# Performance work log

Hardware: AMD Instinct MI355X
Metric: run time of the kernel (lower is better)

Reference implementation:

```python
import jax, jax.numpy as jnp
import numpy as np

T, B, D_IN, D_HID, D_OUT = 512, 64, 512, 512, 512


def setup_inputs() -> dict:
    key = jax.random.key(0)
    k_x, k_xh, k_hh, k_o = jax.random.split(key, 4)
    return {
        "x": jax.random.normal(k_x, (T, B, D_IN), dtype=jnp.float32),
        "xh": jax.random.normal(k_xh, (D_IN, D_HID), dtype=jnp.float32) * 0.01,
        "hh": jax.random.normal(k_hh, (D_HID, D_HID), dtype=jnp.float32) * 0.01,
        "hb": jnp.zeros((D_HID,), dtype=jnp.float32),
        "o": jax.random.normal(k_o, (D_HID, D_OUT), dtype=jnp.float32) * 0.01,
        "h0": jnp.zeros((1, D_HID), dtype=jnp.float32),
    }


def reference(x, xh, hh, hb, o, h0):
    # Elman RNN (training branch): h_t = relu(x_t @ xh + h_{t-1} @ hh + hb); y_t = h_t @ o
    # h starts as (1, hid) and broadcasts to (B, hid) at step 1, as in the torch code.
    batch = x.shape[1]
    h_init = jnp.broadcast_to(h0, (batch, h0.shape[1]))

    def step(h, xi):  # xi: [B, D_IN], h: [B, D_HID]
        h = jax.nn.relu(xi @ xh + h @ hh + hb)
        return h, h @ o  # y: [B, D_OUT]

    _, ys = jax.lax.scan(step, h_init, x)
    return ys  # [T, B, D_OUT] (stacked version of the torch list of outputs)
```

## Files before the change

### kernel.cpp

```cpp
#include <hip/hip_runtime.h>
#include <hip/hip_bf16.h>

#define TSTEPS 512
#define BATCH  64
#define DIM    512
#define NWG    8

using short8 = __attribute__((ext_vector_type(8))) short;
using f32x4  = __attribute__((ext_vector_type(4))) float;

__device__ __forceinline__ unsigned short f2bf(float f) {
    unsigned u = __builtin_bit_cast(unsigned, f);
    unsigned r = (u + 0x7FFFu + ((u >> 16) & 1u)) >> 16;
    return (unsigned short)r;
}

__global__ void conv_oT(const float* __restrict__ src, unsigned short* __restrict__ dst) {
    __shared__ float tile[32][33];
    const int bx = blockIdx.x * 32, by = blockIdx.y * 32;
    const int tx = threadIdx.x & 31, ty = threadIdx.x >> 5;
#pragma unroll
    for (int k = 0; k < 32; k += 8)
        tile[ty + k][tx] = src[(size_t)(by + ty + k) * DIM + bx + tx];
    __syncthreads();
#pragma unroll
    for (int k = 0; k < 32; k += 8)
        dst[(size_t)(bx + ty + k) * DIM + by + tx] = f2bf(tile[tx][ty + k]);
}

__global__ __launch_bounds__(256) void gemm_xw(
    const float* __restrict__ X, const float* __restrict__ W,
    const float* __restrict__ bias, float* __restrict__ Out)
{
    __shared__ float As[16][68];
    __shared__ float Bs[16][68];
    const int tid = threadIdx.x;
    const int m0 = blockIdx.x * 64, n0 = blockIdx.y * 64;
    const int tx = tid & 15, ty = tid >> 4;
    float acc[4][4] = {};
    for (int k0 = 0; k0 < DIM; k0 += 16) {
        {
            int r = tid >> 2, c = (tid & 3) * 4;
            float4 v = *reinterpret_cast<const float4*>(X + (size_t)(m0 + r) * DIM + k0 + c);
            As[c + 0][r] = v.x; As[c + 1][r] = v.y; As[c + 2][r] = v.z; As[c + 3][r] = v.w;
        }
        {
            int r = tid >> 4, c = (tid & 15) * 4;
            float4 v = *reinterpret_cast<const float4*>(W + (size_t)(k0 + r) * DIM + n0 + c);
            Bs[r][c + 0] = v.x; Bs[r][c + 1] = v.y; Bs[r][c + 2] = v.z; Bs[r][c + 3] = v.w;
        }
        __syncthreads();
#pragma unroll
        for (int k = 0; k < 16; ++k) {
            float4 a = *reinterpret_cast<const float4*>(&As[k][ty * 4]);
            float4 b = *reinterpret_cast<const float4*>(&Bs[k][tx * 4]);
            float av[4] = {a.x, a.y, a.z, a.w};
            float bv[4] = {b.x, b.y, b.z, b.w};
#pragma unroll
            for (int i = 0; i < 4; ++i)
#pragma unroll
                for (int j = 0; j < 4; ++j)
                    acc[i][j] = fmaf(av[i], bv[j], acc[i][j]);
        }
        __syncthreads();
    }
    float4 bv = *reinterpret_cast<const float4*>(bias + n0 + tx * 4);
    const float badd[4] = {bv.x, bv.y, bv.z, bv.w};
    float4* Out4 = reinterpret_cast<float4*>(Out);
    const size_t base = (((size_t)blockIdx.x * 4 + (ty & 3)) * 4 + (ty >> 2)) * DIM + n0 + tx * 4;
#pragma unroll
    for (int j = 0; j < 4; ++j) {
        float4 v;
        v.x = acc[0][j] + badd[j]; v.y = acc[1][j] + badd[j];
        v.z = acc[2][j] + badd[j]; v.w = acc[3][j] + badd[j];
        Out4[base + j] = v;
    }
}

__global__ __launch_bounds__(256, 1) void rnn_scan(
    const float* __restrict__ hh, const float* __restrict__ xwb,
    const float* __restrict__ h0, unsigned long long* __restrict__ histU,
    unsigned int* __restrict__ flags)
{
    const int tid  = threadIdx.x;
    const int wg   = blockIdx.x;
    const int lane = tid & 63;
    const int wv   = __builtin_amdgcn_readfirstlane(tid >> 6);
    const int ln15 = lane & 15, kg = lane >> 4;
    const int colw = wg * 64 + wv * 16 + ln15;

    __shared__ unsigned long long hsU[BATCH * DIM / 4];

    short8 Bhh[16];
#pragma unroll
    for (int kk = 0; kk < 16; ++kk) {
        short8 bh;
#pragma unroll
        for (int j = 0; j < 8; ++j) {
            int k = kk * 32 + kg * 8 + j;
            bh[j] = (short)f2bf(hh[(size_t)k * DIM + colw]);
        }
        Bhh[kk] = bh;
    }

    {
        unsigned long long* dst = histU + wv * 2048 + lane;
#pragma unroll 4
        for (int i = 0; i < 32; ++i) {
            float4 f = *reinterpret_cast<const float4*>(h0 + ((i & 1) << 8) + lane * 4);
            unsigned long long v = (unsigned long long)f2bf(f.x)
                | ((unsigned long long)f2bf(f.y) << 16)
                | ((unsigned long long)f2bf(f.z) << 32)
                | ((unsigned long long)f2bf(f.w) << 48);
            __hip_atomic_store(dst + i * 64, v, __ATOMIC_RELAXED, __HIP_MEMORY_SCOPE_AGENT);
        }
    }
    __builtin_amdgcn_fence(__ATOMIC_RELEASE, "agent");
    __syncthreads();

    const float4* xw4 = reinterpret_cast<const float4*>(xwb);
    f32x4 xwr[4];
#pragma unroll
    for (int m = 0; m < 4; ++m) {
        float4 v = xw4[(((size_t)0 * 4 + kg) * 4 + m) * DIM + colw];
        xwr[m] = f32x4{v.x, v.y, v.z, v.w};
    }

    for (int t = 0; t < TSTEPS; ++t) {
        {
            const unsigned long long* src = histU + (size_t)t * 8192 + wv * 2048 + lane;
#pragma unroll
            for (int ii = 0; ii < 32; ii += 8) {
                unsigned long long v[8];
#pragma unroll
                for (int j = 0; j < 8; ++j)
                    v[j] = __hip_atomic_load(src + (ii + j) * 64, __ATOMIC_RELAXED, __HIP_MEMORY_SCOPE_AGENT);
#pragma unroll
                for (int j = 0; j < 8; ++j) {
                    int i = ii + j;
                    int row = (wv << 4) + (i >> 1);
                    int byte = ((row << 10) + ((i & 1) << 9) + (lane << 3)) ^ ((row & 7) << 4);
                    hsU[byte >> 3] = v[j];
                }
            }
        }
        __syncthreads();

        f32x4 acch[4];
#pragma unroll
        for (int m = 0; m < 4; ++m) acch[m] = f32x4{0.f, 0.f, 0.f, 0.f};
#pragma unroll
        for (int kk = 0; kk < 16; ++kk) {
#pragma unroll
            for (int m = 0; m < 4; ++m) {
                int row = m * 16 + ln15;
                int byte = ((row << 10) + (kk << 6) + (kg << 4)) ^ ((row & 7) << 4);
                short8 a = *reinterpret_cast<const short8*>(
                    reinterpret_cast<const char*>(hsU) + byte);
                acch[m] = __builtin_amdgcn_mfma_f32_16x16x32_bf16(a, Bhh[kk], acch[m], 0, 0, 0);
            }
        }

        {
            unsigned short* hdst = reinterpret_cast<unsigned short*>(histU + (size_t)(t + 1) * 8192);
#pragma unroll
            for (int m = 0; m < 4; ++m)
#pragma unroll
                for (int r = 0; r < 4; ++r) {
                    int row = m * 16 + kg * 4 + r;
                    float hn = xwr[m][r] + acch[m][r];
                    hn = hn > 0.f ? hn : 0.f;
                    __hip_atomic_store(hdst + (size_t)row * DIM + colw, f2bf(hn),
                                       __ATOMIC_RELAXED, __HIP_MEMORY_SCOPE_AGENT);
                }
        }
        __builtin_amdgcn_fence(__ATOMIC_RELEASE, "agent");
        __syncthreads();
        if (tid == 0)
            __hip_atomic_store(&flags[wg], (unsigned)(t + 1),
                               __ATOMIC_RELEASE, __HIP_MEMORY_SCOPE_AGENT);

        if (t < TSTEPS - 1) {
#pragma unroll
            for (int m = 0; m < 4; ++m) {
                float4 v = xw4[(((size_t)(t + 1) * 4 + kg) * 4 + m) * DIM + colw];
                xwr[m] = f32x4{v.x, v.y, v.z, v.w};
            }
            if (wv == 0) {
                for (;;) {
                    unsigned f = __hip_atomic_load(&flags[lane & (NWG - 1)],
                                                   __ATOMIC_RELAXED, __HIP_MEMORY_SCOPE_AGENT);
                    if (!__any(f < (unsigned)(t + 1))) break;
                    __builtin_amdgcn_s_sleep(1);
                }
            }
            __syncthreads();
        }
    }
}

__global__ __launch_bounds__(256) void gemm_y(
    const unsigned short* __restrict__ A,
    const unsigned short* __restrict__ Bt,
    float* __restrict__ Out)
{
    __shared__ unsigned short As[128 * 40];
    __shared__ unsigned short Bs[128 * 40];
    const int tid = threadIdx.x;
    const int m0 = blockIdx.x * 128, n0 = blockIdx.y * 128;
    const int lane = tid & 63, wv = tid >> 6;
    const int ln15 = lane & 15, kg = lane >> 4;
    const int wr = (wv >> 1) * 64, wc = (wv & 1) * 64;

    f32x4 acc[4][4];
#pragma unroll
    for (int m = 0; m < 4; ++m)
#pragma unroll
        for (int n = 0; n < 4; ++n) acc[m][n] = f32x4{0.f, 0.f, 0.f, 0.f};

    const int sr = tid & 127;
    for (int k0 = 0; k0 < DIM; k0 += 32) {
        const unsigned short* g = (tid < 128)
            ? A  + (size_t)(m0 + sr) * DIM + k0
            : Bt + (size_t)(n0 + sr) * DIM + k0;
        unsigned short* s = (tid < 128) ? &As[sr * 40] : &Bs[sr * 40];
        ulonglong2 v0 = reinterpret_cast<const ulonglong2*>(g)[0];
        ulonglong2 v1 = reinterpret_cast<const ulonglong2*>(g)[1];
        ulonglong2 v2 = reinterpret_cast<const ulonglong2*>(g)[2];
        ulonglong2 v3 = reinterpret_cast<const ulonglong2*>(g)[3];
        __syncthreads();
        reinterpret_cast<ulonglong2*>(s)[0] = v0;
        reinterpret_cast<ulonglong2*>(s)[1] = v1;
        reinterpret_cast<ulonglong2*>(s)[2] = v2;
        reinterpret_cast<ulonglong2*>(s)[3] = v3;
        __syncthreads();
        short8 af[4], bf[4];
#pragma unroll
        for (int m = 0; m < 4; ++m)
            af[m] = *reinterpret_cast<const short8*>(&As[(wr + m * 16 + ln15) * 40 + kg * 8]);
#pragma unroll
        for (int n = 0; n < 4; ++n)
            bf[n] = *reinterpret_cast<const short8*>(&Bs[(wc + n * 16 + ln15) * 40 + kg * 8]);
#pragma unroll
        for (int m = 0; m < 4; ++m)
#pragma unroll
            for (int n = 0; n < 4; ++n)
                acc[m][n] = __builtin_amdgcn_mfma_f32_16x16x32_bf16(af[m], bf[n], acc[m][n], 0, 0, 0);
    }
#pragma unroll
    for (int m = 0; m < 4; ++m)
#pragma unroll
        for (int n = 0; n < 4; ++n)
#pragma unroll
            for (int r = 0; r < 4; ++r) {
                int row = m0 + wr + m * 16 + kg * 4 + r;
                int col = n0 + wc + n * 16 + ln15;
                Out[(size_t)row * DIM + col] = acc[m][n][r];
            }
}

extern "C" void kernel_launch(void* const* d_in, const int* in_sizes, int n_in,
                              void* d_out, int out_size, void* d_ws, size_t ws_size,
                              hipStream_t stream) {
    const float* x  = (const float*)d_in[0];
    const float* xh = (const float*)d_in[1];
    const float* hh = (const float*)d_in[2];
    const float* hb = (const float*)d_in[3];
    const float* o  = (const float*)d_in[4];
    const float* h0 = (const float*)d_in[5];
    float* out = (float*)d_out;

    unsigned int* flags = (unsigned int*)d_ws;
    unsigned long long* histU = (unsigned long long*)((char*)d_ws + 4096);
    unsigned short* oT = (unsigned short*)((char*)d_ws + 4096 + (size_t)513 * 65536);

    (void)hipMemsetAsync(d_ws, 0, 256, stream);
    conv_oT<<<dim3(16, 16), 256, 0, stream>>>(o, oT);
    gemm_xw<<<dim3(512, 8), 256, 0, stream>>>(x, xh, hb, out);
    rnn_scan<<<NWG, 256, 0, stream>>>(hh, out, h0, histU, flags);
    gemm_y<<<dim3(256, 4), 256, 0, stream>>>(
        (const unsigned short*)histU + 32768, oT, out);
}
```

Baseline: 2.492 ms.

## Use bf16 MFMA for input projection GEMM and relax scan release fences

Replaces the fp32 FMA input-projection GEMM with a 128x128-tile bf16 MFMA kernel, pre-transposing and converting xh to bf16 with the existing transpose kernel. Separately, the recurrent scan swaps agent-scope release fences and the release flag store for an s_waitcnt vmcnt(0) plus a relaxed flag store, to shorten each step's synchronization latency. The GEMM change loses precision on x@xh, and the weaker memory ordering relies on hardware behaviour for cross-workgroup visibility of the hidden-state stores.

```diff
diff --git a/kernel.cpp b/kernel.cpp
--- a/kernel.cpp
+++ b/kernel.cpp
@@ -15,7 +15,7 @@
     return (unsigned short)r;
 }
 
-__global__ void conv_oT(const float* __restrict__ src, unsigned short* __restrict__ dst) {
+__global__ void conv_T(const float* __restrict__ src, unsigned short* __restrict__ dst) {
     __shared__ float tile[32][33];
     const int bx = blockIdx.x * 32, by = blockIdx.y * 32;
     const int tx = threadIdx.x & 31, ty = threadIdx.x >> 5;
@@ -28,52 +28,75 @@
         dst[(size_t)(bx + ty + k) * DIM + by + tx] = f2bf(tile[tx][ty + k]);
 }
 
-__global__ __launch_bounds__(256) void gemm_xw(
-    const float* __restrict__ X, const float* __restrict__ W,
+__global__ __launch_bounds__(256) void gemm_xwm(
+    const float* __restrict__ X,
+    const unsigned short* __restrict__ Bt,
     const float* __restrict__ bias, float* __restrict__ Out)
 {
-    __shared__ float As[16][68];
-    __shared__ float Bs[16][68];
+    __shared__ unsigned short As[128 * 40];
+    __shared__ unsigned short Bs[128 * 40];
     const int tid = threadIdx.x;
-    const int m0 = blockIdx.x * 64, n0 = blockIdx.y * 64;
-    const int tx = tid & 15, ty = tid >> 4;
-    float acc[4][4] = {};
-    for (int k0 = 0; k0 < DIM; k0 += 16) {
+    const int m0 = blockIdx.x * 128, n0 = blockIdx.y * 128;
+    const int lane = tid & 63, wv = tid >> 6;
+    const int ln15 = lane & 15, kg = lane >> 4;
+    const int wr = (wv >> 1) * 64, wc = (wv & 1) * 64;
+
+    f32x4 acc[4][4];
+#pragma unroll
+    for (int m = 0; m < 4; ++m)
+#pragma unroll
+        for (int n = 0; n < 4; ++n) acc[m][n] = f32x4{0.f, 0.f, 0.f, 0.f};
+
+    const int arow = tid >> 1, ahalf = tid & 1;
+    for (int k0 = 0; k0 < DIM; k0 += 32) {
+        const float4* ga = reinterpret_cast<const float4*>(
+            X + (size_t)(m0 + arow) * DIM + k0 + ahalf * 16);
+        float4 a0 = ga[0], a1 = ga[1], a2 = ga[2], a3 = ga[3];
+        const ulonglong2* gb = reinterpret_cast<const ulonglong2*>(
+            Bt + (size_t)(n0 + arow) * DIM + k0 + ahalf * 16);
+        ulonglong2 bv0 = gb[0], bv1 = gb[1];
+        __syncthreads();
         {
-            int r = tid >> 2, c = (tid & 3) * 4;
-            float4 v = *reinterpret_cast<const float4*>(X + (size_t)(m0 + r) * DIM + k0 + c);
-            As[c + 0][r] = v.x; As[c + 1][r] = v.y; As[c + 2][r] = v.z; As[c + 3][r] = v.w;
-        }
-        {
-            int r = tid >> 4, c = (tid & 15) * 4;
-            float4 v = *reinterpret_cast<const float4*>(W + (size_t)(k0 + r) * DIM + n0 + c);
-            Bs[r][c + 0] = v.x; Bs[r][c + 1] = v.y; Bs[r][c + 2] = v.z; Bs[r][c + 3] = v.w;
-        }
-        __syncthreads();
-#pragma unroll
-        for (int k = 0; k < 16; ++k) {
-            float4 a = *reinterpret_cast<const float4*>(&As[k][ty * 4]);
-            float4 b = *reinterpret_cast<const float4*>(&Bs[k][tx * 4]);
-            float av[4] = {a.x, a.y, a.z, a.w};
-            float bv[4] = {b.x, b.y, b.z, b.w};
-#pragma unroll
-            for (int i = 0; i < 4; ++i)
-#pragma unroll
-                for (int j = 0; j < 4; ++j)
-                    acc[i][j] = fmaf(av[i], bv[j], acc[i][j]);
-        }
-        __syncthreads();
-    }
-    float4 bv = *reinterpret_cast<const float4*>(bias + n0 + tx * 4);
-    const float badd[4] = {bv.x, bv.y, bv.z, bv.w};
+            unsigned long long p[4];
+            const float4 av[4] = {a0, a1, a2, a3};
+#pragma unroll
+            for (int q = 0; q < 4; ++q)
+                p[q] = (unsigned long long)f2bf(av[q].x)
+                     | ((unsigned long long)f2bf(av[q].y) << 16)
+                     | ((unsigned long long)f2bf(av[q].z) << 32)
+                     | ((unsigned long long)f2bf(av[q].w) << 48);
+            unsigned long long* s = reinterpret_cast<unsigned long long*>(&As[arow * 40 + ahalf * 16]);
+            s[0] = p[0]; s[1] = p[1]; s[2] = p[2]; s[3] = p[3];
+            *reinterpret_cast<ulonglong2*>(&Bs[arow * 40 + ahalf * 16]) = bv0;
+            *reinterpret_cast<ulonglong2*>(&Bs[arow * 40 + ahalf * 16 + 8]) = bv1;
+        }
+        __syncthreads();
+        short8 af[4], bf[4];
+#pragma unroll
+        for (int m = 0; m < 4; ++m)
+            af[m] = *reinterpret_cast<const short8*>(&As[(wr + m * 16 + ln15) * 40 + kg * 8]);
+#pragma unroll
+        for (int n = 0; n < 4; ++n)
+            bf[n] = *reinterpret_cast<const short8*>(&Bs[(wc + n * 16 + ln15) * 40 + kg * 8]);
+#pragma unroll
+        for (int m = 0; m < 4; ++m)
+#pragma unroll
+            for (int n = 0; n < 4; ++n)
+                acc[m][n] = __builtin_amdgcn_mfma_f32_16x16x32_bf16(af[m], bf[n], acc[m][n], 0, 0, 0);
+    }
     float4* Out4 = reinterpret_cast<float4*>(Out);
-    const size_t base = (((size_t)blockIdx.x * 4 + (ty & 3)) * 4 + (ty >> 2)) * DIM + n0 + tx * 4;
-#pragma unroll
-    for (int j = 0; j < 4; ++j) {
-        float4 v;
-        v.x = acc[0][j] + badd[j]; v.y = acc[1][j] + badd[j];
-        v.z = acc[2][j] + badd[j]; v.w = acc[3][j] + badd[j];
-        Out4[base + j] = v;
+#pragma unroll
+    for (int n = 0; n < 4; ++n) {
+        int col = n0 + wc + n * 16 + ln15;
+        float bb = bias[col];
+#pragma unroll
+        for (int m = 0; m < 4; ++m) {
+            int t = (m0 + wr) >> 6;
+            float4 v;
+            v.x = acc[m][n][0] + bb; v.y = acc[m][n][1] + bb;
+            v.z = acc[m][n][2] + bb; v.w = acc[m][n][3] + bb;
+            Out4[(((size_t)t * 4 + kg) * 4 + m) * DIM + col] = v;
+        }
     }
 }
 
@@ -115,7 +138,7 @@
             __hip_atomic_store(dst + i * 64, v, __ATOMIC_RELAXED, __HIP_MEMORY_SCOPE_AGENT);
         }
     }
-    __builtin_amdgcn_fence(__ATOMIC_RELEASE, "agent");
+    asm volatile("s_waitcnt vmcnt(0)" ::: "memory");
     __syncthreads();
 
     const float4* xw4 = reinterpret_cast<const float4*>(xwb);
@@ -174,11 +197,11 @@
                                        __ATOMIC_RELAXED, __HIP_MEMORY_SCOPE_AGENT);
                 }
         }
-        __builtin_amdgcn_fence(__ATOMIC_RELEASE, "agent");
+        asm volatile("s_waitcnt vmcnt(0)" ::: "memory");
         __syncthreads();
         if (tid == 0)
             __hip_atomic_store(&flags[wg], (unsigned)(t + 1),
-                               __ATOMIC_RELEASE, __HIP_MEMORY_SCOPE_AGENT);
+                               __ATOMIC_RELAXED, __HIP_MEMORY_SCOPE_AGENT);
 
         if (t < TSTEPS - 1) {
 #pragma unroll
@@ -272,11 +295,13 @@
 
     unsigned int* flags = (unsigned int*)d_ws;
     unsigned long long* histU = (unsigned long long*)((char*)d_ws + 4096);
-    unsigned short* oT = (unsigned short*)((char*)d_ws + 4096 + (size_t)513 * 65536);
+    unsigned short* oT  = (unsigned short*)((char*)d_ws + 4096 + (size_t)513 * 65536);
+    unsigned short* xhT = oT + (size_t)DIM * DIM;
 
     (void)hipMemsetAsync(d_ws, 0, 256, stream);
-    conv_oT<<<dim3(16, 16), 256, 0, stream>>>(o, oT);
-    gemm_xw<<<dim3(512, 8), 256, 0, stream>>>(x, xh, hb, out);
+    conv_T<<<dim3(16, 16), 256, 0, stream>>>(o, oT);
+    conv_T<<<dim3(16, 16), 256, 0, stream>>>(xh, xhT);
+    gemm_xwm<<<dim3(256, 4), 256, 0, stream>>>(x, xhT, hb, out);
     rnn_scan<<<NWG, 256, 0, stream>>>(hh, out, h0, histU, flags);
     gemm_y<<<dim3(256, 4), 256, 0, stream>>>(
         (const unsigned short*)histU + 32768, oT, out);
```

Result: faster. 2.154 ms (-13.6%).
